# Optimization experiments

Hardware: AMD Instinct MI355X
Metric: run time of the kernel (lower is better)

Reference implementation:

```python
import jax, jax.numpy as jnp
import numpy as np

N = 100000      # nodes
E = 3200000     # edges (avg degree 32)
F_IN = 16       # data.num_features
H = 16          # hidden width (hard-coded in module)
C = 2           # data.num_classes
N_MID = 5       # conv2..conv6


def setup_inputs() -> dict:
    key = jax.random.key(0)
    ks = jax.random.split(key, 12)
    s = lambda fan_in: 1.0 / np.sqrt(fan_in)
    x = jax.random.normal(ks[0], (N, F_IN), jnp.float32)
    edge_index = jax.random.randint(ks[1], (2, E), 0, N, jnp.int32)
    return {
        "x": x,
        "edge_index": edge_index,
        "Wl1": jax.random.normal(ks[2], (F_IN, H), jnp.float32) * s(F_IN),
        "Wr1": jax.random.normal(ks[3], (F_IN, H), jnp.float32) * s(F_IN),
        "b1": jnp.zeros((H,), jnp.float32),
        "Wl_mid": jax.random.normal(ks[4], (N_MID, H, H), jnp.float32) * s(H),
        "Wr_mid": jax.random.normal(ks[5], (N_MID, H, H), jnp.float32) * s(H),
        "b_mid": jnp.zeros((N_MID, H), jnp.float32),
        "Wl7": jax.random.normal(ks[6], (H, C), jnp.float32) * s(H),
        "Wr7": jax.random.normal(ks[7], (H, C), jnp.float32) * s(H),
        "b7": jnp.zeros((C,), jnp.float32),
    }


def _sage_conv(x, src, dst, Wl, bl, Wr):
    # PyG SAGEConv(aggr='max'): out = lin_l(max_j x_j) + lin_r(x_i)
    msg = x[src]                                  # [E, F] neighbor gather
    agg = jax.ops.segment_max(msg, dst, num_segments=N)
    agg = jnp.where(jnp.isfinite(agg), agg, 0.0)  # isolated nodes -> 0
    return agg @ Wl + bl + x @ Wr


def reference(x, edge_index, Wl1, Wr1, b1, Wl_mid, Wr_mid, b_mid, Wl7, Wr7, b7):
    src, dst = edge_index[0], edge_index[1]
    h = jax.nn.relu(_sage_conv(x, src, dst, Wl1, b1, Wr1))
    for i in range(N_MID):
        h = jax.nn.relu(_sage_conv(h, src, dst, Wl_mid[i], b_mid[i], Wr_mid[i]))
    # F.dropout with training=False (inference) is identity
    h = _sage_conv(h, src, dst, Wl7, b7, Wr7)
    return jax.nn.log_softmax(h, axis=1)
```

## Files before the change

### kernel.cpp

```cpp
#include <hip/hip_runtime.h>
#include <hip/hip_fp16.h>

#define N_NODES 100000
#define N_EDGES 3200000
#define HDIM 16
#define NB 391
#define P1_BLOCKS 256
#define P1_THREADS 1024
#define P1_EPB 12500
#define SLOT 64
#define BSTRIDE (P1_BLOCKS * SLOT)
#define SENT 0xFBFFFBFFu

typedef unsigned u32;

__device__ __forceinline__ u32 pkmax(u32 a, u32 b) {
    u32 r;
    asm("v_pk_max_f16 %0, %1, %2" : "=v"(r) : "v"(a), "v"(b));
    return r;
}
__device__ __forceinline__ float2 h2f2(u32 u) {
    __half2 h = *reinterpret_cast<__half2*>(&u);
    return __half22float2(h);
}
__device__ __forceinline__ u32 f2h2(float a, float b) {
    __half2 h = __float22half2_rn(make_float2(a, b));
    return *reinterpret_cast<u32*>(&h);
}


__global__ __launch_bounds__(P1_THREADS)
void pass1_bucket(const int* __restrict__ src, const int* __restrict__ dst,
                  u32* __restrict__ priv, int* __restrict__ cnt,
                  const float4* __restrict__ x, uint2* __restrict__ h0) {
    __shared__ int lh[NB];
    int t = threadIdx.x;
    int blk = blockIdx.x;

    {
        int ci = blk * P1_THREADS + t;
        if (ci < N_NODES * HDIM / 4) {
            float4 v = x[ci];
            h0[ci] = make_uint2(f2h2(v.x, v.y), f2h2(v.z, v.w));
        }
        int ci2 = ci + P1_BLOCKS * P1_THREADS;
        if (ci2 < N_NODES * HDIM / 4) {
            float4 v = x[ci2];
            h0[ci2] = make_uint2(f2h2(v.x, v.y), f2h2(v.z, v.w));
        }
        if (blk == 0 && t < 8)
            ((u32*)h0)[(size_t)N_NODES * 8 + t] = SENT;
    }

    for (int i = t; i < NB; i += P1_THREADS) lh[i] = 0;
    __syncthreads();

    int e0 = blk * P1_EPB;
    int n = min(P1_EPB, N_EDGES - e0);
    for (int j = t; j < n; j += P1_THREADS) {
        int d = dst[e0 + j];
        int s = src[e0 + j];
        int bk = d >> 8;
        u32 pv = (u32)s | ((u32)(d & 255) << 17);
        int r = atomicAdd(&lh[bk], 1);
        if (r < SLOT)
            priv[(size_t)bk * BSTRIDE + blk * SLOT + r] = pv;
    }
    __syncthreads();
    for (int i = t; i < NB; i += P1_THREADS)
        cnt[i * P1_BLOCKS + blk] = min(lh[i], SLOT);
}


__global__ __launch_bounds__(1024)
void pass2_sort(u32* __restrict__ priv, const int* __restrict__ cnt,
                int2* __restrict__ row2) {
    __shared__ int sdeg[256], spd[256], ssc[256], scnt[256];
    __shared__ int colst[13312];
    __shared__ int stot;
    int t = threadIdx.x;
    int b = blockIdx.x;
    size_t base = (size_t)b * BSTRIDE;
    int node0 = b << 8;
    int nn = min(256, N_NODES - node0);

    if (t < 256) { sdeg[t] = 0; scnt[t] = cnt[b * P1_BLOCKS + t]; }
    __syncthreads();

    u32 vv[16];
    int rr[16];
#pragma unroll
    for (int k = 0; k < 16; ++k) {
        int idx = k * 1024 + t;
        int s = idx >> 6, sl = idx & 63;
        rr[k] = -1;
        if (sl < scnt[s]) {
            u32 v = priv[base + idx];
            vv[k] = v;
            rr[k] = atomicAdd(&sdeg[v >> 17], 1);
        }
    }
    __syncthreads();
    if (t < 256) {
        int d = sdeg[t];
        int pd = (d + 15) & ~15;
        spd[t] = pd;
        ssc[t] = pd;
    }
    __syncthreads();
    for (int off = 1; off < 256; off <<= 1) {
        int u = 0;
        if (t < 256 && t >= off) u = ssc[t - off];
        __syncthreads();
        if (t < 256) ssc[t] += u;
        __syncthreads();
    }
    if (t < 256) {
        int ex = ssc[t] - spd[t];
        ssc[t] = ex;
        if (t < nn) row2[node0 + t] = make_int2((int)base + ex, (int)base + ex + spd[t]);
        if (t == 255) stot = ex + spd[t];
        for (int q = ex + sdeg[t]; q < ex + spd[t]; ++q)
            colst[q] = N_NODES;
    }
    __syncthreads();
#pragma unroll
    for (int k = 0; k < 16; ++k) {
        if (rr[k] >= 0)
            colst[ssc[vv[k] >> 17] + rr[k]] = vv[k] & 0x1FFFF;
    }
    __syncthreads();
    int tot = stot;
    for (int j = t; j < tot; j += 1024) priv[base + j] = (unsigned)colst[j];
    if (t < 48) priv[base + tot + t] = N_NODES;
}


template <int HOUT, bool RELU, bool LSM>
__global__ void sage_layer(const u32* __restrict__ h,
                           const int2* __restrict__ row2,
                           const unsigned* __restrict__ col,
                           const float* __restrict__ Wl,
                           const float* __restrict__ Wr,
                           const float* __restrict__ b,
                           void* __restrict__ out) {
    __shared__ float sWl[HDIM * HOUT];
    __shared__ float sWr[HDIM * HOUT];
    __shared__ float sb[HOUT];
    int t = threadIdx.x;
    if (t < HDIM * HOUT) { sWl[t] = Wl[t]; sWr[t] = Wr[t]; }
    if (t < HOUT) sb[t] = b[t];
    if (HOUT == 16) {
        if (blockIdx.x == 0 && t < 8)
            ((u32*)out)[(size_t)N_NODES * 8 + t] = SENT;
    }

    int nl = t >> 3, g = t & 7, p = g >> 1, hf = g & 1;
    int i = blockIdx.x * 32 + nl;

    int2 r2 = row2[i];
    int beg = r2.x, endp = r2.y;
    const uint4* h4 = (const uint4*)h;
    const unsigned* cp = col + 4 * p;

    uint4 xr = h4[i * 2 + hf];

    uint4 cc = *(const uint4*)(cp + beg);
    uint4 nc = *(const uint4*)(cp + beg + 16);
    uint4 v0 = h4[(int)cc.x * 2 + hf];
    uint4 v1 = h4[(int)cc.y * 2 + hf];
    uint4 v2 = h4[(int)cc.z * 2 + hf];
    uint4 v3 = h4[(int)cc.w * 2 + hf];

    u32 a0 = SENT, a1 = SENT, a2 = SENT, a3 = SENT;
    for (int j = beg; j < endp; j += 16) {
        uint4 w0 = h4[(int)nc.x * 2 + hf];
        uint4 w1 = h4[(int)nc.y * 2 + hf];
        uint4 w2 = h4[(int)nc.z * 2 + hf];
        uint4 w3 = h4[(int)nc.w * 2 + hf];
        uint4 nc2 = *(const uint4*)(cp + j + 32);
        a0 = pkmax(a0, pkmax(pkmax(v0.x, v1.x), pkmax(v2.x, v3.x)));
        a1 = pkmax(a1, pkmax(pkmax(v0.y, v1.y), pkmax(v2.y, v3.y)));
        a2 = pkmax(a2, pkmax(pkmax(v0.z, v1.z), pkmax(v2.z, v3.z)));
        a3 = pkmax(a3, pkmax(pkmax(v0.w, v1.w), pkmax(v2.w, v3.w)));
        v0 = w0; v1 = w1; v2 = w2; v3 = w3;
        nc = nc2;
    }
#pragma unroll
    for (int m = 2; m <= 4; m <<= 1) {
        a0 = pkmax(a0, (u32)__shfl_xor((int)a0, m));
        a1 = pkmax(a1, (u32)__shfl_xor((int)a1, m));
        a2 = pkmax(a2, (u32)__shfl_xor((int)a2, m));
        a3 = pkmax(a3, (u32)__shfl_xor((int)a3, m));
    }
    if (beg == endp) { a0 = a1 = a2 = a3 = 0u; }

    float fa[8], fx[8];
    {
        float2 f;
        f = h2f2(a0);   fa[0] = f.x; fa[1] = f.y;
        f = h2f2(a1);   fa[2] = f.x; fa[3] = f.y;
        f = h2f2(a2);   fa[4] = f.x; fa[5] = f.y;
        f = h2f2(a3);   fa[6] = f.x; fa[7] = f.y;
        f = h2f2(xr.x); fx[0] = f.x; fx[1] = f.y;
        f = h2f2(xr.y); fx[2] = f.x; fx[3] = f.y;
        f = h2f2(xr.z); fx[4] = f.x; fx[5] = f.y;
        f = h2f2(xr.w); fx[6] = f.x; fx[7] = f.y;
    }
    int fb = hf * 8;

    __syncthreads();

    if (HOUT == 16) {
        float o0 = 0.f, o1 = 0.f, o2 = 0.f, o3 = 0.f;
#pragma unroll
        for (int q = 0; q < 8; ++q) {
            int f = fb + q;
            float4 wl = ((const float4*)sWl)[f * 4 + p];
            float4 wr = ((const float4*)sWr)[f * 4 + p];
            o0 += fa[q] * wl.x + fx[q] * wr.x;
            o1 += fa[q] * wl.y + fx[q] * wr.y;
            o2 += fa[q] * wl.z + fx[q] * wr.z;
            o3 += fa[q] * wl.w + fx[q] * wr.w;
        }
        o0 += __shfl_xor(o0, 1);
        o1 += __shfl_xor(o1, 1);
        o2 += __shfl_xor(o2, 1);
        o3 += __shfl_xor(o3, 1);
        if (hf == 0) {
            int c0 = p * 4;
            o0 += sb[c0]; o1 += sb[c0 + 1]; o2 += sb[c0 + 2]; o3 += sb[c0 + 3];
            if (RELU) {
                o0 = fmaxf(o0, 0.f); o1 = fmaxf(o1, 0.f);
                o2 = fmaxf(o2, 0.f); o3 = fmaxf(o3, 0.f);
            }
            ((uint2*)out)[i * 4 + p] = make_uint2(f2h2(o0, o1), f2h2(o2, o3));
        }
    } else {
        float o0 = 0.f, o1 = 0.f;
#pragma unroll
        for (int q = 0; q < 8; ++q) {
            int f = fb + q;
            o0 += fa[q] * sWl[f * 2 + 0] + fx[q] * sWr[f * 2 + 0];
            o1 += fa[q] * sWl[f * 2 + 1] + fx[q] * sWr[f * 2 + 1];
        }
        o0 += __shfl_xor(o0, 1);
        o1 += __shfl_xor(o1, 1);
        if (g == 0) {
            o0 += sb[0]; o1 += sb[1];
            if (LSM) {
                float m = fmaxf(o0, o1);
                float lse = m + logf(expf(o0 - m) + expf(o1 - m));
                o0 -= lse; o1 -= lse;
            }
            ((float2*)out)[i] = make_float2(o0, o1);
        }
    }
}


extern "C" void kernel_launch(void* const* d_in, const int* in_sizes, int n_in,
                              void* d_out, int out_size, void* d_ws, size_t ws_size,
                              hipStream_t stream) {
    const float* x      = (const float*)d_in[0];
    const int*   ei     = (const int*)d_in[1];
    const float* Wl1    = (const float*)d_in[2];
    const float* Wr1    = (const float*)d_in[3];
    const float* b1     = (const float*)d_in[4];
    const float* Wl_mid = (const float*)d_in[5];
    const float* Wr_mid = (const float*)d_in[6];
    const float* b_mid  = (const float*)d_in[7];
    const float* Wl7    = (const float*)d_in[8];
    const float* Wr7    = (const float*)d_in[9];
    const float* b7     = (const float*)d_in[10];
    float* out = (float*)d_out;

    const int* src = ei;
    const int* dst = ei + N_EDGES;

    char* ws = (char*)d_ws;
    size_t off = 0;
    auto alloc = [&](size_t bytes) {
        void* p = ws + off;
        off += (bytes + 255) & ~(size_t)255;
        return p;
    };
    u32*  priv = (u32*)alloc((size_t)NB * BSTRIDE * 4);
    int*  cnt  = (int*)alloc((size_t)NB * P1_BLOCKS * 4);
    int2* row2 = (int2*)alloc((size_t)N_NODES * 8);
    u32*  h0   = (u32*)alloc((size_t)(N_NODES + 1) * HDIM * 2);
    u32*  hA   = (u32*)alloc((size_t)(N_NODES + 1) * HDIM * 2);
    u32*  hB   = (u32*)alloc((size_t)(N_NODES + 1) * HDIM * 2);

    dim3 bL((N_NODES + 31) / 32);

    pass1_bucket<<<P1_BLOCKS, P1_THREADS, 0, stream>>>(src, dst, priv, cnt,
                                                       (const float4*)x, (uint2*)h0);
    pass2_sort<<<NB, 1024, 0, stream>>>(priv, cnt, row2);

    sage_layer<16, true, false><<<bL, 256, 0, stream>>>(h0, row2, priv, Wl1, Wr1, b1, hA);

    u32* cur = hA;
    u32* nxt = hB;
    for (int i = 0; i < 5; ++i) {
        sage_layer<16, true, false><<<bL, 256, 0, stream>>>(
            cur, row2, priv, Wl_mid + i * 256, Wr_mid + i * 256, b_mid + i * 16, nxt);
        u32* tmp = cur; cur = nxt; nxt = tmp;
    }

    sage_layer<2, false, true><<<bL, 256, 0, stream>>>(cur, row2, priv, Wl7, Wr7, b7, out);
}
```

Before: 191.2 us.

## Stage bucketed edges in LDS before coalesced writes to private slots

The edge bucketing pass now works in two halves. Each half counts per-bucket occupancy, runs a prefix scan over padded counts, packs the edges into an LDS staging buffer grouped by bucket, and then writes them out contiguously per bucket. The aim is to replace scattered single-word global stores with more coalesced bursts. The cost is extra barriers, a 512-wide scan done twice, and much higher LDS use, which may reduce occupancy in pass1.

```diff
diff --git a/kernel.cpp b/kernel.cpp
--- a/kernel.cpp
+++ b/kernel.cpp
@@ -8,6 +8,7 @@
 #define P1_BLOCKS 256
 #define P1_THREADS 1024
 #define P1_EPB 12500
+#define P1_HALF 6250
 #define SLOT 64
 #define BSTRIDE (P1_BLOCKS * SLOT)
 #define SENT 0xFBFFFBFFu
@@ -34,6 +35,10 @@
                   u32* __restrict__ priv, int* __restrict__ cnt,
                   const float4* __restrict__ x, uint2* __restrict__ h0) {
     __shared__ int lh[NB];
+    __shared__ int cum[NB];
+    __shared__ int pexcl[512];
+    __shared__ unsigned short c2b[1152];
+    __shared__ u32 staged[8992];
     int t = threadIdx.x;
     int blk = blockIdx.x;
 
@@ -52,23 +57,75 @@
             ((u32*)h0)[(size_t)N_NODES * 8 + t] = SENT;
     }
 
-    for (int i = t; i < NB; i += P1_THREADS) lh[i] = 0;
-    __syncthreads();
-
-    int e0 = blk * P1_EPB;
-    int n = min(P1_EPB, N_EDGES - e0);
-    for (int j = t; j < n; j += P1_THREADS) {
-        int d = dst[e0 + j];
-        int s = src[e0 + j];
-        int bk = d >> 8;
-        u32 pv = (u32)s | ((u32)(d & 255) << 17);
-        int r = atomicAdd(&lh[bk], 1);
-        if (r < SLOT)
-            priv[(size_t)bk * BSTRIDE + blk * SLOT + r] = pv;
-    }
-    __syncthreads();
+    for (int i = t; i < NB; i += P1_THREADS) cum[i] = 0;
+
+    for (int half = 0; half < 2; ++half) {
+        for (int i = t; i < NB; i += P1_THREADS) lh[i] = 0;
+        __syncthreads();
+
+        int e0 = blk * P1_EPB + half * P1_HALF;
+        u32 vv[7];
+        int br[7];
+#pragma unroll
+        for (int k = 0; k < 7; ++k) {
+            int j = k * P1_THREADS + t;
+            br[k] = -1;
+            if (j < P1_HALF) {
+                int d = dst[e0 + j];
+                int s = src[e0 + j];
+                int bk = d >> 8;
+                vv[k] = (u32)s | ((u32)(d & 255) << 17);
+                int r = atomicAdd(&lh[bk], 1);
+                br[k] = (r << 9) | bk;
+            }
+        }
+        __syncthreads();
+
+        int pc = 0;
+        if (t < 512) {
+            pc = (t < NB) ? ((lh[t] + 7) & ~7) : 0;
+            pexcl[t] = pc;
+        }
+        __syncthreads();
+        for (int off = 1; off < 512; off <<= 1) {
+            int u = 0;
+            if (t < 512 && t >= off) u = pexcl[t - off];
+            __syncthreads();
+            if (t < 512) pexcl[t] += u;
+            __syncthreads();
+        }
+        if (t < NB) {
+            int ex = pexcl[t] - pc;
+            for (int c = ex >> 3; c < (pexcl[t] >> 3); ++c)
+                c2b[c] = (unsigned short)t;
+        }
+#pragma unroll
+        for (int k = 0; k < 7; ++k) {
+            if (br[k] >= 0) {
+                int bk = br[k] & 511;
+                int r = br[k] >> 9;
+                int ex = pexcl[bk] - ((lh[bk] + 7) & ~7);
+                staged[ex + r] = vv[k];
+            }
+        }
+        __syncthreads();
+
+        int tot = pexcl[511];
+        for (int j = t; j < tot; j += P1_THREADS) {
+            int bk = c2b[j >> 3];
+            int ex = pexcl[bk] - ((lh[bk] + 7) & ~7);
+            int off2 = j - ex;
+            int base = cum[bk];
+            if (off2 < lh[bk] && base + off2 < SLOT)
+                priv[(size_t)bk * BSTRIDE + blk * SLOT + base + off2] = staged[j];
+        }
+        __syncthreads();
+        for (int i = t; i < NB; i += P1_THREADS) cum[i] += lh[i];
+        __syncthreads();
+    }
+
     for (int i = t; i < NB; i += P1_THREADS)
-        cnt[i * P1_BLOCKS + blk] = min(lh[i], SLOT);
+        cnt[i * P1_BLOCKS + blk] = min(cum[i], SLOT);
 }
 
 
```

After: 188.8 us (median of 2 runs). No clear change (-1.3%).
